# Kernel tuning notes

Hardware: AMD Instinct MI355X
Metric: run time of the kernel (lower is better)

Reference implementation:

```python
import jax, jax.numpy as jnp
import numpy as np

B, C, H, W = 8, 256, 64, 64
NH, D = 4, 64
BLKQ = BLKK = 64
TOPK_RATIO = 0.1
EPS = 1e-6


def setup_inputs() -> dict:
    key = jax.random.key(0)
    k1, k2, k3, k4, k5 = jax.random.split(key, 5)
    x = jax.random.normal(k1, (B, C, H, W), dtype=jnp.float32)
    qkv_w = jax.random.normal(k2, (3 * C, C), dtype=jnp.float32) / np.sqrt(C)
    out_w = jax.random.normal(k3, (C, C), dtype=jnp.float32) / np.sqrt(C)
    # NOTE: the torch module zero-inits proj_l and out_proj (output would be
    # identically zero); we use small random weights for a useful baseline.
    proj_lw = jax.random.normal(k4, (D, D), dtype=jnp.float32) * 0.02
    proj_lb = jax.random.normal(k5, (D,), dtype=jnp.float32) * 0.02
    return {"x": x, "qkv_w": qkv_w, "out_w": out_w, "proj_lw": proj_lw, "proj_lb": proj_lb}


def _sla_forward(x, qkv_w, out_w, proj_lw, proj_lb):
    Bn, Cn, Hn, Wn = x.shape
    L = Hn * Wn
    nQ, nK = L // BLKQ, L // BLKK
    T = max(1, int(TOPK_RATIO * nK))  # real_topk = 6
    xf = x.reshape(Bn, Cn, L)
    qkv = jnp.einsum('oc,bcl->bol', qkv_w, xf)  # 1x1 conv, no bias
    q, k, v = jnp.split(qkv, 3, axis=1)
    # (B, C, L) -> (B, H, L, D)
    def to_bhld(t):
        return t.reshape(Bn, NH, D, L).transpose(0, 1, 3, 2)
    q, k, v = to_bhld(q), to_bhld(k), to_bhld(v)

    # ---- block-level top-k map (get_block_map) ----
    qr = q.reshape(Bn, NH, nQ, BLKQ, D)
    kr = k.reshape(Bn, NH, nK, BLKK, D)
    vr = v.reshape(Bn, NH, nK, BLKK, D)
    qb = qr.mean(axis=3)                       # (B,H,nQ,D)
    kb = kr.mean(axis=3)                       # (B,H,nK,D)
    blk_scores = jnp.einsum('bhnd,bhmd->bhnm', qb, kb)
    _, lut = jax.lax.top_k(blk_scores, T)      # (B,H,nQ,T)

    # ---- sparse path: softmax attention over gathered top-k key blocks ----
    idx = lut[..., None, None]                 # (B,H,nQ,T,1,1)
    kg = jnp.take_along_axis(kr[:, :, None], idx, axis=3)  # (B,H,nQ,T,BLKK,D)
    vg = jnp.take_along_axis(vr[:, :, None], idx, axis=3)
    kg = kg.reshape(Bn, NH, nQ, T * BLKK, D)
    vg = vg.reshape(Bn, NH, nQ, T * BLKK, D)
    scale = D ** -0.5
    s = jnp.einsum('bhnqd,bhnkd->bhnqk', qr, kg) * scale
    p = jax.nn.softmax(s, axis=-1)
    o_s = jnp.einsum('bhnqk,bhnkd->bhnqd', p, vg)          # (B,H,nQ,BLKQ,D)

    # ---- linear path over complement (non-selected) key blocks ----
    c_q = jax.nn.softmax(q, axis=-1)           # feature_map='softmax'
    c_k = jax.nn.softmax(k, axis=-1)
    c_kr = c_k.reshape(Bn, NH, nK, BLKK, D)
    kvb = jnp.einsum('bhmkd,bhmke->bhmde', c_kr, vr)       # (B,H,nK,D,D)
    ksum = c_kr.sum(axis=3)                                # (B,H,nK,D)
    sel = jax.nn.one_hot(lut, nK, dtype=q.dtype).sum(axis=3)  # (B,H,nQ,nK)
    comp = 1.0 - sel
    kv_q = jnp.einsum('bhnm,bhmde->bhnde', comp, kvb)
    ks_q = jnp.einsum('bhnm,bhmd->bhnd', comp, ksum)
    c_qr = c_q.reshape(Bn, NH, nQ, BLKQ, D)
    num = jnp.einsum('bhnqd,bhnde->bhnqe', c_qr, kv_q)
    den = jnp.einsum('bhnqd,bhnd->bhnq', c_qr, ks_q)
    o_l = num / (den[..., None] + EPS)

    o_l = jnp.einsum('bhnqd,ed->bhnqe', o_l, proj_lw) + proj_lb
    o = (o_s + o_l).reshape(Bn, NH, L, D)
    o = o.transpose(0, 1, 3, 2).reshape(Bn, Cn, L)
    o = jnp.einsum('oc,bcl->bol', out_w, o)    # out_proj 1x1 conv
    return o.reshape(Bn, Cn, Hn, Wn)


def reference(x, qkv_w, out_w, proj_lw, proj_lb):
    return _sla_forward(x, qkv_w, out_w, proj_lw, proj_lb)
```

## Files before the change

### kernel.cpp

```cpp
#include <hip/hip_runtime.h>
#include <hip/hip_bf16.h>
#include <cmath>

#define NB 8
#define NC 256
#define NHH 4
#define DD 64
#define LL 4096
#define NQ 64
#define NKB 64
#define BLK 64
#define TT 6
#define PAD 72

typedef _Float16 f16;
typedef _Float16 half8 __attribute__((ext_vector_type(8)));
typedef float f32x4 __attribute__((ext_vector_type(4)));
typedef unsigned int uint4v __attribute__((ext_vector_type(4)));
typedef unsigned long long ull;

#define INV2048 4.8828125e-4f

union H4 { f16 h[4]; ull u; };
union H2 { f16 h[2]; unsigned int u; };

#define MFMA16(A, B, C) __builtin_amdgcn_mfma_f32_16x16x32_f16(A, B, C, 0, 0, 0)

__global__ void qbkb_kernel(const float* __restrict__ w, const float* __restrict__ xb,
                            float* __restrict__ qb, float* __restrict__ kb) {
  int id = blockIdx.x;
  int h = id % NHH; id /= NHH;
  int n = id % NQ;  int b = id / NQ;
  int t = threadIdx.x;
  int d = t & 63;
  int part = t >> 6;
  const float* wrow = w + (size_t)(part * NC + h * DD + d) * NC;
  const float* xcol = xb + (size_t)b * NC * NQ + n;
  float acc = 0.f;
#pragma unroll 4
  for (int c = 0; c < NC; ++c) acc += wrow[c] * xcol[(size_t)c * NQ];
  float* dst = (part == 0) ? qb : kb;
  dst[(((size_t)b * NHH + h) * NQ + n) * DD + d] = acc;
}

__global__ void topk_kernel(const float* __restrict__ qb, const float* __restrict__ kb,
                            int* __restrict__ lut) {
  __shared__ float kbs[NKB][DD + 1];
  int id = blockIdx.x;
  int n = id % NQ;
  int bh = id / NQ;
  int m = threadIdx.x;
  const float* kbp = kb + (size_t)bh * NKB * DD;
  for (int i = threadIdx.x; i < NKB * DD; i += 64) kbs[i >> 6][i & 63] = kbp[i];
  __syncthreads();
  const float* qrow = qb + ((size_t)bh * NQ + n) * DD;
  float s = 0.f;
#pragma unroll 8
  for (int d2 = 0; d2 < DD; ++d2) s += qrow[d2] * kbs[m][d2];
  for (int t = 0; t < TT; ++t) {
    float v = s; int i = m;
#pragma unroll
    for (int off = 1; off < 64; off <<= 1) {
      float ov = __shfl_xor(v, off);
      int oi = __shfl_xor(i, off);
      if (ov > v || (ov == v && oi < i)) { v = ov; i = oi; }
    }
    if (m == 0) lut[(size_t)id * TT + t] = i;
    if (m == i) s = -INFINITY;
  }
}

__global__ void wsplit_kernel(const float* __restrict__ wq, const float* __restrict__ wo,
                              const float* __restrict__ plw,
                              f16* __restrict__ wqh,
                              f16* __restrict__ woh, f16* __restrict__ wol,
                              f16* __restrict__ plwh, f16* __restrict__ plwl) {
  int blk = blockIdx.x;
  if (blk < 192) {
    int i = (blk * 256 + threadIdx.x) * 4;
    float4 v = *(const float4*)(wq + i);
    H4 hh;
    hh.h[0] = (f16)v.x; hh.h[1] = (f16)v.y; hh.h[2] = (f16)v.z; hh.h[3] = (f16)v.w;
    *(ull*)(wqh + i) = hh.u;
    return;
  }
  const float* src; f16* dh; f16* dl; int n;
  if (blk < 256) { src = wo;  dh = woh;  dl = wol;  n = NC * NC; blk -= 192; }
  else           { src = plw; dh = plwh; dl = plwl; n = DD * DD; blk -= 256; }
  int i = (blk * 256 + threadIdx.x) * 4;
  if (i >= n) return;
  float4 v = *(const float4*)(src + i);
  H4 hh, ll;
  hh.h[0] = (f16)v.x; ll.h[0] = (f16)((v.x - (float)hh.h[0]) * 2048.f);
  hh.h[1] = (f16)v.y; ll.h[1] = (f16)((v.y - (float)hh.h[1]) * 2048.f);
  hh.h[2] = (f16)v.z; ll.h[2] = (f16)((v.z - (float)hh.h[2]) * 2048.f);
  hh.h[3] = (f16)v.w; ll.h[3] = (f16)((v.w - (float)hh.h[3]) * 2048.f);
  *(ull*)(dh + i) = hh.u;
  *(ull*)(dl + i) = ll.u;
}

__global__ __launch_bounds__(256) void xsplit_kernel(const float* __restrict__ x,
                                                     f16* __restrict__ xh,
                                                     float* __restrict__ xb) {
  __shared__ float T[64][65];
  int l0 = blockIdx.x * 64, c0 = blockIdx.y * 64, b = blockIdx.z;
  int tid = threadIdx.x;
  for (int it = 0; it < 16; ++it) {
    int idx = it * 256 + tid; int c = idx >> 6, l = idx & 63;
    T[c][l] = x[((size_t)b * NC + c0 + c) * LL + l0 + l];
  }
  __syncthreads();
  {
    int c = tid >> 2, qq = tid & 3;
    float s = 0.f;
#pragma unroll
    for (int l = 0; l < 16; ++l) s += T[c][qq * 16 + l];
    s += __shfl_xor(s, 1);
    s += __shfl_xor(s, 2);
    if (qq == 0) xb[((size_t)b * NC + c0 + c) * NQ + blockIdx.x] = s * (1.f / 64.f);
  }
  for (int it = 0; it < 4; ++it) {
    int idx = it * 256 + tid; int l = idx >> 4, cq = idx & 15;
    H4 hh;
    hh.h[0] = (f16)T[cq * 4 + 0][l];
    hh.h[1] = (f16)T[cq * 4 + 1][l];
    hh.h[2] = (f16)T[cq * 4 + 2][l];
    hh.h[3] = (f16)T[cq * 4 + 3][l];
    *(ull*)(xh + ((size_t)b * LL + l0 + l) * NC + c0 + cq * 4) = hh.u;
  }
}

__global__ __launch_bounds__(256, 8) void q_mfma(
    const f16* __restrict__ xh,
    const f16* __restrict__ wh,
    f16* __restrict__ qh) {
  __shared__ f16 XH[BLK][PAD];
  int L = blockIdx.x;
  int b = L & 7;
  int t = L >> 3;
  int l0 = (t >> 2) * 64;
  int h = t & 3;
  int tid = threadIdx.x;
  int w = tid >> 6, lane = tid & 63, c16 = lane & 15, g = lane >> 4;
  f32x4 acc[4];
#pragma unroll
  for (int j = 0; j < 4; ++j) acc[j] = (f32x4){0.f,0.f,0.f,0.f};
  size_t wbase = (size_t)(h * DD + w * 16 + c16) * NC;
  for (int c0 = 0; c0 < NC; c0 += 64) {
    __syncthreads();
#pragma unroll
    for (int it = 0; it < 2; ++it) {
      int idx = it * 256 + tid; int pos = idx >> 3, dp8 = idx & 7;
      size_t gsrc = ((size_t)b * LL + l0 + pos) * NC + c0 + dp8 * 8;
      *(uint4v*)&XH[pos][dp8 * 8] = *(const uint4v*)(xh + gsrc);
    }
    __syncthreads();
#pragma unroll
    for (int ks = 0; ks < 2; ++ks) {
      half8 awh = *(const half8*)(wh + wbase + c0 + ks * 32 + g * 8);
#pragma unroll
      for (int j = 0; j < 4; ++j) {
        half8 bxh = *(const half8*)&XH[j * 16 + c16][ks * 32 + g * 8];
        acc[j] = MFMA16(awh, bxh, acc[j]);
      }
    }
  }
#pragma unroll
  for (int j = 0; j < 4; ++j) {
    H4 hh;
#pragma unroll
    for (int r = 0; r < 4; ++r) hh.h[r] = (f16)acc[j][r];
    size_t off = (((size_t)b * NHH + h) * LL + l0 + j * 16 + c16) * DD + w * 16 + g * 4;
    *(ull*)(qh + off) = hh.u;
  }
}

__global__ __launch_bounds__(256, 8) void kv_mfma(
    const f16* __restrict__ xh,
    const f16* __restrict__ wh,
    f16* __restrict__ kh, f16* __restrict__ vT) {
  __shared__ f16 XH[BLK][PAD];
  int L = blockIdx.x;
  int b = L & 7;
  int t = L >> 3;
  int l0 = (t >> 2) * 64;
  int h = t & 3;
  int tid = threadIdx.x;
  int w = tid >> 6, lane = tid & 63, c16 = lane & 15, g = lane >> 4;
  f32x4 acck[4], accv[4];
#pragma unroll
  for (int j = 0; j < 4; ++j) { acck[j] = (f32x4){0.f,0.f,0.f,0.f}; accv[j] = (f32x4){0.f,0.f,0.f,0.f}; }
  size_t wkbase = (size_t)(NC + h * DD + w * 16 + c16) * NC;
  size_t wvbase = (size_t)(2 * NC + h * DD + w * 16 + c16) * NC;
  for (int c0 = 0; c0 < NC; c0 += 64) {
    __syncthreads();
#pragma unroll
    for (int it = 0; it < 2; ++it) {
      int idx = it * 256 + tid; int pos = idx >> 3, dp8 = idx & 7;
      size_t gsrc = ((size_t)b * LL + l0 + pos) * NC + c0 + dp8 * 8;
      *(uint4v*)&XH[pos][dp8 * 8] = *(const uint4v*)(xh + gsrc);
    }
    __syncthreads();
#pragma unroll
    for (int ks = 0; ks < 2; ++ks) {
      half8 awk = *(const half8*)(wh + wkbase + c0 + ks * 32 + g * 8);
      half8 awv = *(const half8*)(wh + wvbase + c0 + ks * 32 + g * 8);
#pragma unroll
      for (int j = 0; j < 4; ++j) {
        half8 bxh = *(const half8*)&XH[j * 16 + c16][ks * 32 + g * 8];
        acck[j] = MFMA16(awk, bxh, acck[j]);
        accv[j] = MFMA16(awv, bxh, accv[j]);
      }
    }
  }
#pragma unroll
  for (int j = 0; j < 4; ++j) {
    H4 hk;
#pragma unroll
    for (int r = 0; r < 4; ++r) hk.h[r] = (f16)acck[j][r];
    size_t off = (((size_t)b * NHH + h) * LL + l0 + j * 16 + c16) * DD + w * 16 + g * 4;
    *(ull*)(kh + off) = hk.u;
  }
  __syncthreads();
#pragma unroll
  for (int j = 0; j < 4; ++j)
#pragma unroll
    for (int r = 0; r < 4; ++r)
      XH[j * 16 + c16][w * 16 + g * 4 + r] = (f16)accv[j][r];
  __syncthreads();
  int bh = b * NHH + h;
#pragma unroll
  for (int it = 0; it < 4; ++it) {
    int idx = it * 256 + tid; int d = idx >> 4, p4 = (idx & 15) * 4;
    H4 hh;
    hh.h[0] = XH[p4 + 0][d]; hh.h[1] = XH[p4 + 1][d];
    hh.h[2] = XH[p4 + 2][d]; hh.h[3] = XH[p4 + 3][d];
    *(ull*)(vT + ((size_t)bh * DD + d) * LL + l0 + p4) = hh.u;
  }
}

__global__ __launch_bounds__(256) void kvb_kernel(
    const f16* __restrict__ khg, const f16* __restrict__ vT,
    f16* __restrict__ kvbT, float* __restrict__ ksum) {
  __shared__ float ck[BLK][DD + 1];
  __shared__ float vsT[BLK][DD + 4];
  int id = blockIdx.x;
  int m = id % NKB;
  int bh = id / NKB;
  int tid = threadIdx.x;
  int r = tid >> 2, p = tid & 3;
  {
    size_t base = ((size_t)bh * LL + (size_t)m * BLK + r) * DD + p * 16;
    half8 a = *(const half8*)(khg + base), a2 = *(const half8*)(khg + base + 8);
#pragma unroll
    for (int c = 0; c < 8; ++c) {
      ck[r][p * 16 + c] = (float)a[c];
      ck[r][p * 16 + 8 + c] = (float)a2[c];
    }
  }
#pragma unroll
  for (int it = 0; it < 2; ++it) {
    int idx = it * 256 + tid; int e = idx >> 3, c8 = idx & 7;
    half8 vv = *(const half8*)(vT + ((size_t)bh * DD + e) * LL + (size_t)m * BLK + c8 * 8);
#pragma unroll
    for (int c = 0; c < 8; ++c) vsT[e][c8 * 8 + c] = (float)vv[c];
  }
  __syncthreads();
  {
    float mx = -INFINITY;
#pragma unroll
    for (int c = 0; c < 16; ++c) mx = fmaxf(mx, ck[r][p * 16 + c]);
    mx = fmaxf(mx, __shfl_xor(mx, 1));
    mx = fmaxf(mx, __shfl_xor(mx, 2));
    float e[16]; float sum = 0.f;
#pragma unroll
    for (int c = 0; c < 16; ++c) { e[c] = __expf(ck[r][p * 16 + c] - mx); sum += e[c]; }
    sum += __shfl_xor(sum, 1);
    sum += __shfl_xor(sum, 2);
    float inv = 1.0f / sum;
#pragma unroll
    for (int c = 0; c < 16; ++c) ck[r][p * 16 + c] = e[c] * inv;
  }
  __syncthreads();
  if (tid < DD) {
    float s = 0.f;
#pragma unroll 8
    for (int j = 0; j < BLK; ++j) s += ck[j][tid];
    ksum[((size_t)bh * NKB + m) * DD + tid] = s;
  }
  int tx = tid & 15, ty = tid >> 4;
  float acc[4][4] = {};
#pragma unroll 4
  for (int j = 0; j < BLK; ++j) {
    float a[4], bb[4];
#pragma unroll
    for (int i = 0; i < 4; ++i) a[i] = vsT[ty * 4 + i][j];
#pragma unroll
    for (int jj = 0; jj < 4; ++jj) bb[jj] = ck[j][tx * 4 + jj];
#pragma unroll
    for (int i = 0; i < 4; ++i)
#pragma unroll
      for (int jj = 0; jj < 4; ++jj) acc[i][jj] += a[i] * bb[jj];
  }
  f16* dst = kvbT + ((size_t)bh * NKB + m) * DD * DD;
#pragma unroll
  for (int i = 0; i < 4; ++i) {
    H4 hh;
#pragma unroll
    for (int jj = 0; jj < 4; ++jj) hh.h[jj] = (f16)acc[i][jj];
    *(ull*)(dst + (size_t)(ty * 4 + i) * DD + tx * 4) = hh.u;
  }
}

__global__ void totals_kernel(const f16* __restrict__ kvbT, const float* __restrict__ ksum,
                              float* __restrict__ kvtot, float* __restrict__ kstot) {
  int bi = blockIdx.x;
  int bh = bi >> 4, s = bi & 15;
  int tid = threadIdx.x;
  int i = s * 256 + tid;
  float acc = 0.f;
  const f16* src = kvbT + (size_t)bh * NKB * DD * DD + i;
  for (int m2 = 0; m2 < NKB; ++m2) acc += (float)src[(size_t)m2 * DD * DD];
  kvtot[(size_t)bh * DD * DD + i] = acc;
  if (s == 0 && tid < DD) {
    float ss = 0.f;
    for (int m2 = 0; m2 < NKB; ++m2) ss += ksum[((size_t)bh * NKB + m2) * DD + tid];
    kstot[(size_t)bh * DD + tid] = ss;
  }
}

__global__ __launch_bounds__(256) void attn_mfma(
    const f16* __restrict__ qh_g,
    const f16* __restrict__ kh_g, const f16* __restrict__ vT_g,
    const f16* __restrict__ kvbT, const float* __restrict__ ksum,
    const float* __restrict__ kvtot, const float* __restrict__ kstot,
    const int* __restrict__ lut,
    const f16* __restrict__ plwh, const f16* __restrict__ plwl,
    const float* __restrict__ plb,
    f16* __restrict__ och) {
  __shared__ f16 KH[BLK][PAD], VH[BLK][PAD], PH[BLK][PAD];
  __shared__ float ksq[DD], dinv[BLK];
  int L = blockIdx.x;
  int rest = L >> 3;
  int bh = (L & 7) * 4 + (rest >> 6);
  int n = rest & 63;
  int id = bh * NQ + n;
  int b = bh >> 2, h = bh & 3;
  int tid = threadIdx.x;
  int w = tid >> 6, lane = tid & 63, c16 = lane & 15, g = lane >> 4;
  int lu[TT];
#pragma unroll
  for (int t = 0; t < TT; ++t) lu[t] = lut[(size_t)id * TT + t];
  size_t qbase = ((size_t)bh * LL + (size_t)n * BLK + w * 16 + c16) * DD;
  half8 bqh[2];
#pragma unroll
  for (int ks = 0; ks < 2; ++ks) bqh[ks] = *(const half8*)(qh_g + qbase + ks * 32 + g * 8);
  f32x4 acco[4];
#pragma unroll
  for (int j = 0; j < 4; ++j) acco[j] = (f32x4){0.f,0.f,0.f,0.f};
  float l_run = 0.f;
  uint4v kreg[2], vreg[2];
  {
    int mb = lu[0];
#pragma unroll
    for (int it = 0; it < 2; ++it) {
      int idx = it * 256 + tid; int pos = idx >> 3, dp8 = idx & 7;
      kreg[it] = *(const uint4v*)(kh_g + ((size_t)bh * LL + (size_t)mb * BLK + pos) * DD + dp8 * 8);
      vreg[it] = *(const uint4v*)(vT_g + ((size_t)bh * DD + pos) * LL + (size_t)mb * BLK + dp8 * 8);
    }
  }
  for (int t = 0; t < TT; ++t) {
    __syncthreads();
#pragma unroll
    for (int it = 0; it < 2; ++it) {
      int idx = it * 256 + tid; int pos = idx >> 3, dp8 = idx & 7;
      *(uint4v*)&KH[pos][dp8 * 8] = kreg[it];
      *(uint4v*)&VH[pos][dp8 * 8] = vreg[it];
    }
    __syncthreads();
    if (t + 1 < TT) {
      int mb = lu[t + 1];
#pragma unroll
      for (int it = 0; it < 2; ++it) {
        int idx = it * 256 + tid; int pos = idx >> 3, dp8 = idx & 7;
        kreg[it] = *(const uint4v*)(kh_g + ((size_t)bh * LL + (size_t)mb * BLK + pos) * DD + dp8 * 8);
        vreg[it] = *(const uint4v*)(vT_g + ((size_t)bh * DD + pos) * LL + (size_t)mb * BLK + dp8 * 8);
      }
    }
    float rs = 0.f;
#pragma unroll
    for (int i = 0; i < 4; ++i) {
      f32x4 acc = {0.f, 0.f, 0.f, 0.f};
#pragma unroll
      for (int ks = 0; ks < 2; ++ks) {
        half8 ah = *(const half8*)&KH[i * 16 + c16][ks * 32 + g * 8];
        acc = MFMA16(ah, bqh[ks], acc);
      }
      H4 pp;
#pragma unroll
      for (int r = 0; r < 4; ++r) {
        float p = __expf(acc[r] * 0.125f - 4.f);
        rs += p;
        pp.h[r] = (f16)p;
      }
      *(ull*)&PH[w * 16 + c16][i * 16 + g * 4] = pp.u;
    }
    rs += __shfl_xor(rs, 16);
    rs += __shfl_xor(rs, 32);
    l_run += rs;
#pragma unroll
    for (int ks = 0; ks < 2; ++ks) {
      half8 pb = *(const half8*)&PH[w * 16 + c16][ks * 32 + g * 8];
#pragma unroll
      for (int j = 0; j < 4; ++j) {
        half8 vhf = *(const half8*)&VH[j * 16 + c16][ks * 32 + g * 8];
        acco[j] = MFMA16(vhf, pb, acco[j]);
      }
    }
  }
  __syncthreads();
  float linv = 1.f / l_run;
#pragma unroll
  for (int j = 0; j < 4; ++j)
#pragma unroll
    for (int r = 0; r < 4; ++r) acco[j][r] *= linv;
  if (tid < DD) {
    float s = kstot[(size_t)bh * DD + tid];
#pragma unroll
    for (int t2 = 0; t2 < TT; ++t2) s -= ksum[((size_t)bh * NKB + lu[t2]) * DD + tid];
    ksq[tid] = s;
  }
  int cr = tid >> 2, cp = tid & 3;
  float cq[16];
  {
    size_t qrow = ((size_t)bh * LL + (size_t)n * BLK + cr) * DD + cp * 16;
    half8 qa = *(const half8*)(qh_g + qrow), qa2 = *(const half8*)(qh_g + qrow + 8);
#pragma unroll
    for (int c = 0; c < 8; ++c) {
      cq[c] = (float)qa[c];
      cq[8 + c] = (float)qa2[c];
    }
    float mx2 = -INFINITY;
#pragma unroll
    for (int c = 0; c < 16; ++c) mx2 = fmaxf(mx2, cq[c]);
    mx2 = fmaxf(mx2, __shfl_xor(mx2, 1));
    mx2 = fmaxf(mx2, __shfl_xor(mx2, 2));
    float sum = 0.f;
#pragma unroll
    for (int c = 0; c < 16; ++c) { cq[c] = __expf(cq[c] - mx2); sum += cq[c]; }
    sum += __shfl_xor(sum, 1);
    sum += __shfl_xor(sum, 2);
    float inv = 1.f / sum;
#pragma unroll
    for (int c = 0; c < 16; ++c) cq[c] *= inv;
  }
#pragma unroll
  for (int c = 0; c < 8; ++c) {
    H2 hh, ll;
    hh.h[0] = (f16)cq[2 * c];     ll.h[0] = (f16)((cq[2 * c] - (float)hh.h[0]) * 2048.f);
    hh.h[1] = (f16)cq[2 * c + 1]; ll.h[1] = (f16)((cq[2 * c + 1] - (float)hh.h[1]) * 2048.f);
    *(unsigned int*)&VH[cr][cp * 16 + 2 * c] = hh.u;
    *(unsigned int*)&PH[cr][cp * 16 + 2 * c] = ll.u;
  }
  {
    const float* kvtp = kvtot + (size_t)bh * DD * DD;
    const f16* kvbp = kvbT + (size_t)bh * NKB * DD * DD;
    for (int it = 0; it < 16; ++it) {
      int idx = it * 256 + tid;
      int dd2 = idx & 63, e = idx >> 6;
      float s = kvtp[e * DD + dd2];
#pragma unroll
      for (int t2 = 0; t2 < TT; ++t2)
        s -= (float)kvbp[(size_t)lu[t2] * DD * DD + e * DD + dd2];
      KH[e][dd2] = (f16)s;
    }
  }
  __syncthreads();
  {
    float dpart = 0.f;
#pragma unroll
    for (int c = 0; c < 16; ++c) dpart += cq[c] * ksq[cp * 16 + c];
    dpart += __shfl_xor(dpart, 1);
    dpart += __shfl_xor(dpart, 2);
    if (cp == 0) dinv[cr] = 1.f / (dpart + 1e-6f);
  }
  f32x4 accn[4], accn2[4];
  {
    half8 cqh[2], cql[2];
#pragma unroll
    for (int ks = 0; ks < 2; ++ks) {
      cqh[ks] = *(const half8*)&VH[w * 16 + c16][ks * 32 + g * 8];
      cql[ks] = *(const half8*)&PH[w * 16 + c16][ks * 32 + g * 8];
    }
#pragma unroll
    for (int j = 0; j < 4; ++j) {
      f32x4 acc = {0.f, 0.f, 0.f, 0.f};
      f32x4 accc = {0.f, 0.f, 0.f, 0.f};
#pragma unroll
      for (int ks = 0; ks < 2; ++ks) {
        half8 ah = *(const half8*)&KH[j * 16 + c16][ks * 32 + g * 8];
        acc  = MFMA16(ah, cqh[ks], acc);
        accc = MFMA16(ah, cql[ks], accc);
      }
      accn[j] = acc; accn2[j] = accc;
    }
  }
  __syncthreads();
  float di = dinv[w * 16 + c16];
#pragma unroll
  for (int j = 0; j < 4; ++j) {
    float o0 = (accn[j][0] + accn2[j][0] * INV2048) * di;
    float o1 = (accn[j][1] + accn2[j][1] * INV2048) * di;
    float o2 = (accn[j][2] + accn2[j][2] * INV2048) * di;
    float o3 = (accn[j][3] + accn2[j][3] * INV2048) * di;
    H4 hh, ll;
    hh.h[0] = (f16)o0; ll.h[0] = (f16)((o0 - (float)hh.h[0]) * 2048.f);
    hh.h[1] = (f16)o1; ll.h[1] = (f16)((o1 - (float)hh.h[1]) * 2048.f);
    hh.h[2] = (f16)o2; ll.h[2] = (f16)((o2 - (float)hh.h[2]) * 2048.f);
    hh.h[3] = (f16)o3; ll.h[3] = (f16)((o3 - (float)hh.h[3]) * 2048.f);
    *(ull*)&PH[w * 16 + c16][j * 16 + g * 4] = hh.u;
    *(ull*)&KH[w * 16 + c16][j * 16 + g * 4] = ll.u;
  }
  f32x4 accf2[4];
#pragma unroll
  for (int j = 0; j < 4; ++j) accf2[j] = (f32x4){0.f,0.f,0.f,0.f};
#pragma unroll
  for (int ks = 0; ks < 2; ++ks) {
    half8 bolh = *(const half8*)&PH[w * 16 + c16][ks * 32 + g * 8];
    half8 boll = *(const half8*)&KH[w * 16 + c16][ks * 32 + g * 8];
#pragma unroll
    for (int j = 0; j < 4; ++j) {
      size_t pwoff = (size_t)(j * 16 + c16) * DD + ks * 32 + g * 8;
      half8 awh = *(const half8*)(plwh + pwoff);
      half8 awl = *(const half8*)(plwl + pwoff);
      acco[j]  = MFMA16(awh, bolh, acco[j]);
      accf2[j] = MFMA16(awh, boll, accf2[j]);
      accf2[j] = MFMA16(awl, bolh, accf2[j]);
    }
  }
  size_t obase = ((size_t)b * LL + (size_t)n * BLK + w * 16 + c16) * NC + h * DD;
#pragma unroll
  for (int j = 0; j < 4; ++j) {
    H4 hh;
#pragma unroll
    for (int r = 0; r < 4; ++r) {
      int e2 = j * 16 + g * 4 + r;
      hh.h[r] = (f16)(acco[j][r] + accf2[j][r] * INV2048 + plb[e2]);
    }
    *(ull*)(och + obase + j * 16 + g * 4) = hh.u;
  }
}

__global__ __launch_bounds__(256) void out_mfma(
    const f16* __restrict__ och,
    const f16* __restrict__ wh, const f16* __restrict__ wl,
    float* __restrict__ out) {
  __shared__ f16 OH[BLK][PAD];
  int l0 = blockIdx.x * 64;
  int o0 = blockIdx.y * 64;
  int b = blockIdx.z;
  int tid = threadIdx.x;
  int w = tid >> 6, lane = tid & 63, c16 = lane & 15, g = lane >> 4;
  f32x4 acc[4], acc2[4];
#pragma unroll
  for (int j = 0; j < 4; ++j) { acc[j] = (f32x4){0.f,0.f,0.f,0.f}; acc2[j] = (f32x4){0.f,0.f,0.f,0.f}; }
  size_t wbase = (size_t)(o0 + w * 16 + c16) * NC;
  for (int c0 = 0; c0 < NC; c0 += 64) {
    __syncthreads();
#pragma unroll
    for (int it = 0; it < 2; ++it) {
      int idx = it * 256 + tid; int pos = idx >> 3, dp8 = idx & 7;
      size_t gsrc = ((size_t)b * LL + l0 + pos) * NC + c0 + dp8 * 8;
      *(uint4v*)&OH[pos][dp8 * 8] = *(const uint4v*)(och + gsrc);
    }
    __syncthreads();
#pragma unroll
    for (int ks = 0; ks < 2; ++ks) {
      half8 awh = *(const half8*)(wh + wbase + c0 + ks * 32 + g * 8);
      half8 awl = *(const half8*)(wl + wbase + c0 + ks * 32 + g * 8);
#pragma unroll
      for (int j = 0; j < 4; ++j) {
        half8 bh = *(const half8*)&OH[j * 16 + c16][ks * 32 + g * 8];
        acc[j]  = MFMA16(awh, bh, acc[j]);
        acc2[j] = MFMA16(awl, bh, acc2[j]);
      }
    }
  }
#pragma unroll
  for (int j = 0; j < 4; ++j)
#pragma unroll
    for (int r = 0; r < 4; ++r)
      out[((size_t)b * NC + o0 + w * 16 + g * 4 + r) * LL + l0 + j * 16 + c16] =
          acc[j][r] + acc2[j][r] * INV2048;
}

extern "C" void kernel_launch(void* const* d_in, const int* in_sizes, int n_in,
                              void* d_out, int out_size, void* d_ws, size_t ws_size,
                              hipStream_t stream) {
  (void)in_sizes; (void)n_in; (void)out_size; (void)ws_size;
  const float* x = (const float*)d_in[0];
  const float* qkv_w = (const float*)d_in[1];
  const float* out_w = (const float*)d_in[2];
  const float* plw = (const float*)d_in[3];
  const float* plb = (const float*)d_in[4];
  float* out = (float*)d_out;
  const size_t E = (size_t)NB * NHH * LL * DD;
  f16* fb = (f16*)d_ws;
  f16* qh = fb;
  f16* kh = qh + E;
  f16* vT = kh + E;
  f16* xTh = vT + E;
  f16* och = xTh;
  f16* kvbT = xTh + E;
  float* fbase = (float*)(kvbT + E);
  float* ksum = fbase;
  float* kvtot = ksum + (size_t)NB * NHH * NKB * DD;
  float* kstot = kvtot + (size_t)NB * NHH * DD * DD;
  float* xb = kstot + (size_t)NB * NHH * DD;
  float* qb = xb + (size_t)NB * NC * NQ;
  float* kb = qb + (size_t)NB * NHH * NQ * DD;
  int* lut = (int*)(kb + (size_t)NB * NHH * NQ * DD);
  f16* wqh = (f16*)(lut + (size_t)NB * NHH * NQ * TT);
  f16* woh = wqh + (size_t)3 * NC * NC;
  f16* wol = woh + (size_t)NC * NC;
  f16* plwh = wol + (size_t)NC * NC;
  f16* plwl = plwh + (size_t)DD * DD;

  xsplit_kernel<<<dim3(LL / 64, NC / 64, NB), 256, 0, stream>>>(x, xTh, xb);
  qbkb_kernel<<<NB * NQ * NHH, 128, 0, stream>>>(qkv_w, xb, qb, kb);
  topk_kernel<<<NB * NHH * NQ, 64, 0, stream>>>(qb, kb, lut);
  wsplit_kernel<<<260, 256, 0, stream>>>(qkv_w, out_w, plw, wqh, woh, wol, plwh, plwl);
  q_mfma<<<LL / 64 * NHH * NB, 256, 0, stream>>>(xTh, wqh, qh);
  kv_mfma<<<LL / 64 * NHH * NB, 256, 0, stream>>>(xTh, wqh, kh, vT);
  kvb_kernel<<<NB * NHH * NKB, 256, 0, stream>>>(kh, vT, kvbT, ksum);
  totals_kernel<<<NB * NHH * 16, 256, 0, stream>>>(kvbT, ksum, kvtot, kstot);
  attn_mfma<<<NB * NHH * NQ, 256, 0, stream>>>(qh, kh, vT, kvbT, ksum,
                                               kvtot, kstot, lut, plwh, plwl, plb,
                                               och);
  out_mfma<<<dim3(LL / 64, NC / 64, NB), 256, 0, stream>>>(och, woh, wol, out);
}
```

Before: 200.4 us.

## Fuse per-block KV summary computation into kv_mfma projection kernel

Folds the kvb_kernel (softmax feature map on K, per-block ksum and K^T V outer products) into the epilogue of kv_mfma, reusing the K and V tiles already held in shared memory. This removes one kernel launch and the global re-read of K and V for each block. In exchange the fused kernel uses more shared memory (a second f16 tile) and stores the softmaxed K in f16 instead of f32, which slightly lowers precision and may cut occupancy below the declared 8 blocks.

```diff
diff --git a/kernel.cpp b/kernel.cpp
--- a/kernel.cpp
+++ b/kernel.cpp
@@ -178,13 +178,16 @@
 __global__ __launch_bounds__(256, 8) void kv_mfma(
     const f16* __restrict__ xh,
     const f16* __restrict__ wh,
-    f16* __restrict__ kh, f16* __restrict__ vT) {
+    f16* __restrict__ kh, f16* __restrict__ vT,
+    f16* __restrict__ kvbT, float* __restrict__ ksum) {
   __shared__ f16 XH[BLK][PAD];
+  __shared__ f16 VS[BLK][PAD];
   int L = blockIdx.x;
   int b = L & 7;
   int t = L >> 3;
   int l0 = (t >> 2) * 64;
   int h = t & 3;
+  int m = l0 >> 6;
   int tid = threadIdx.x;
   int w = tid >> 6, lane = tid & 63, c16 = lane & 15, g = lane >> 4;
   f32x4 acck[4], accv[4];
@@ -213,90 +216,65 @@
       }
     }
   }
+  int bh = b * NHH + h;
 #pragma unroll
   for (int j = 0; j < 4; ++j) {
     H4 hk;
 #pragma unroll
     for (int r = 0; r < 4; ++r) hk.h[r] = (f16)acck[j][r];
-    size_t off = (((size_t)b * NHH + h) * LL + l0 + j * 16 + c16) * DD + w * 16 + g * 4;
+    size_t off = ((size_t)bh * LL + l0 + j * 16 + c16) * DD + w * 16 + g * 4;
     *(ull*)(kh + off) = hk.u;
   }
   __syncthreads();
 #pragma unroll
   for (int j = 0; j < 4; ++j)
 #pragma unroll
-    for (int r = 0; r < 4; ++r)
-      XH[j * 16 + c16][w * 16 + g * 4 + r] = (f16)accv[j][r];
-  __syncthreads();
-  int bh = b * NHH + h;
+    for (int r = 0; r < 4; ++r) {
+      XH[j * 16 + c16][w * 16 + g * 4 + r] = (f16)acck[j][r];
+      VS[j * 16 + c16][w * 16 + g * 4 + r] = (f16)accv[j][r];
+    }
+  __syncthreads();
 #pragma unroll
   for (int it = 0; it < 4; ++it) {
     int idx = it * 256 + tid; int d = idx >> 4, p4 = (idx & 15) * 4;
     H4 hh;
-    hh.h[0] = XH[p4 + 0][d]; hh.h[1] = XH[p4 + 1][d];
-    hh.h[2] = XH[p4 + 2][d]; hh.h[3] = XH[p4 + 3][d];
+    hh.h[0] = VS[p4 + 0][d]; hh.h[1] = VS[p4 + 1][d];
+    hh.h[2] = VS[p4 + 2][d]; hh.h[3] = VS[p4 + 3][d];
     *(ull*)(vT + ((size_t)bh * DD + d) * LL + l0 + p4) = hh.u;
   }
-}
-
-__global__ __launch_bounds__(256) void kvb_kernel(
-    const f16* __restrict__ khg, const f16* __restrict__ vT,
-    f16* __restrict__ kvbT, float* __restrict__ ksum) {
-  __shared__ float ck[BLK][DD + 1];
-  __shared__ float vsT[BLK][DD + 4];
-  int id = blockIdx.x;
-  int m = id % NKB;
-  int bh = id / NKB;
-  int tid = threadIdx.x;
-  int r = tid >> 2, p = tid & 3;
   {
-    size_t base = ((size_t)bh * LL + (size_t)m * BLK + r) * DD + p * 16;
-    half8 a = *(const half8*)(khg + base), a2 = *(const half8*)(khg + base + 8);
-#pragma unroll
-    for (int c = 0; c < 8; ++c) {
-      ck[r][p * 16 + c] = (float)a[c];
-      ck[r][p * 16 + 8 + c] = (float)a2[c];
-    }
-  }
-#pragma unroll
-  for (int it = 0; it < 2; ++it) {
-    int idx = it * 256 + tid; int e = idx >> 3, c8 = idx & 7;
-    half8 vv = *(const half8*)(vT + ((size_t)bh * DD + e) * LL + (size_t)m * BLK + c8 * 8);
-#pragma unroll
-    for (int c = 0; c < 8; ++c) vsT[e][c8 * 8 + c] = (float)vv[c];
-  }
-  __syncthreads();
-  {
+    int r = tid >> 2, p = tid & 3;
+    float v[16];
     float mx = -INFINITY;
 #pragma unroll
-    for (int c = 0; c < 16; ++c) mx = fmaxf(mx, ck[r][p * 16 + c]);
+    for (int c = 0; c < 16; ++c) { v[c] = (float)XH[r][p * 16 + c]; mx = fmaxf(mx, v[c]); }
     mx = fmaxf(mx, __shfl_xor(mx, 1));
     mx = fmaxf(mx, __shfl_xor(mx, 2));
-    float e[16]; float sum = 0.f;
-#pragma unroll
-    for (int c = 0; c < 16; ++c) { e[c] = __expf(ck[r][p * 16 + c] - mx); sum += e[c]; }
+    float sum = 0.f;
+#pragma unroll
+    for (int c = 0; c < 16; ++c) { v[c] = __expf(v[c] - mx); sum += v[c]; }
     sum += __shfl_xor(sum, 1);
     sum += __shfl_xor(sum, 2);
     float inv = 1.0f / sum;
 #pragma unroll
-    for (int c = 0; c < 16; ++c) ck[r][p * 16 + c] = e[c] * inv;
+    for (int c = 0; c < 16; ++c) XH[r][p * 16 + c] = (f16)(v[c] * inv);
   }
   __syncthreads();
   if (tid < DD) {
     float s = 0.f;
 #pragma unroll 8
-    for (int j = 0; j < BLK; ++j) s += ck[j][tid];
+    for (int j = 0; j < BLK; ++j) s += (float)XH[j][tid];
     ksum[((size_t)bh * NKB + m) * DD + tid] = s;
   }
   int tx = tid & 15, ty = tid >> 4;
   float acc[4][4] = {};
 #pragma unroll 4
   for (int j = 0; j < BLK; ++j) {
+    H4 va = *(H4*)&VS[j][ty * 4];
+    H4 ca = *(H4*)&XH[j][tx * 4];
     float a[4], bb[4];
 #pragma unroll
-    for (int i = 0; i < 4; ++i) a[i] = vsT[ty * 4 + i][j];
-#pragma unroll
-    for (int jj = 0; jj < 4; ++jj) bb[jj] = ck[j][tx * 4 + jj];
+    for (int i = 0; i < 4; ++i) { a[i] = (float)va.h[i]; bb[i] = (float)ca.h[i]; }
 #pragma unroll
     for (int i = 0; i < 4; ++i)
 #pragma unroll
@@ -631,8 +609,7 @@
   topk_kernel<<<NB * NHH * NQ, 64, 0, stream>>>(qb, kb, lut);
   wsplit_kernel<<<260, 256, 0, stream>>>(qkv_w, out_w, plw, wqh, woh, wol, plwh, plwl);
   q_mfma<<<LL / 64 * NHH * NB, 256, 0, stream>>>(xTh, wqh, qh);
-  kv_mfma<<<LL / 64 * NHH * NB, 256, 0, stream>>>(xTh, wqh, kh, vT);
-  kvb_kernel<<<NB * NHH * NKB, 256, 0, stream>>>(kh, vT, kvbT, ksum);
+  kv_mfma<<<LL / 64 * NHH * NB, 256, 0, stream>>>(xTh, wqh, kh, vT, kvbT, ksum);
   totals_kernel<<<NB * NHH * 16, 256, 0, stream>>>(kvbT, ksum, kvtot, kstot);
   attn_mfma<<<NB * NHH * NQ, 256, 0, stream>>>(qh, kh, vT, kvbT, ksum,
                                                kvtot, kstot, lut, plwh, plwl, plb,
```

Measured after the change: 190.1 us. -5.1%, faster.
